# Optimization experiments

Measured on AMD Instinct MI355X. Metric: run time of the kernel, lower is better.

Reference implementation:

```python
import jax, jax.numpy as jnp
import numpy as np

B, NWORD, HID = 4, 24, 512


def setup_inputs() -> dict:
    key = jax.random.key(0)
    ks = jax.random.split(key, 7)
    H = HID
    scale_in = 1.0 / np.sqrt(H)
    return {
        "seqt": jax.random.normal(ks[0], (B, NWORD, 2 * H), dtype=jnp.float32),
        # ins_input_linearity: Linear(H -> 5H) with bias
        "Wi": jax.random.normal(ks[1], (5 * H, H), dtype=jnp.float32) * scale_in,
        "bi": jnp.zeros((5 * H,), dtype=jnp.float32),
        # ins_state_linearity: Linear(H -> 5H) with bias (bias init: forget slots = 1)
        "Ws": jax.random.normal(ks[2], (5 * H, H), dtype=jnp.float32) * scale_in,
        "bs": jnp.zeros((5 * H,), dtype=jnp.float32).at[H:2 * H].set(1.0),
        # ins_bilinearity: BilinearSimilarity(2H, 2H) -> scalar x^T W y
        "Wbil": jax.random.normal(ks[3], (2 * H, 2 * H), dtype=jnp.float32) * (1.0 / (2.0 * H)),
    }


def reference(seqt, Wi, bi, Ws, bs, Wbil):
    """Inside pass (do_inside) of DioLstm in training mode (soft_sum over splits).

    Chart cell (left, L) covers words [left, left+L]. Returns root v = concat(h, c).
    """
    Bn, n, twoH = seqt.shape
    H = twoH // 2
    # ins_bias buffer: ones on the two forget-gate slots [H:3H]
    ins_bias = jnp.zeros((5 * H,), dtype=seqt.dtype).at[H:3 * H].set(1.0)

    def single(seq):  # seq: [n, 2H]
        chartH = jnp.zeros((n, n, H), seq.dtype).at[:, 0].set(seq[:, :H])
        chartC = jnp.zeros((n, n, H), seq.dtype).at[:, 0].set(seq[:, H:])
        chartS = jnp.zeros((n, n), seq.dtype)  # leaf scores are 0
        for L in range(1, n):  # span length - 1 (static unroll over diagonals)
            P = n - L  # number of spans on this diagonal
            lefts = jnp.arange(P)[:, None]          # [P,1]
            ksplit = jnp.arange(L)[None, :]          # [1,L]
            # left child: (left, k); right child: (left+k+1, L-1-k)
            lH = chartH[lefts, ksplit]; lC = chartC[lefts, ksplit]; lS = chartS[lefts, ksplit]
            ridx = lefts + ksplit + 1
            rlen = jnp.broadcast_to(L - 1 - ksplit, ridx.shape)
            rH = chartH[ridx, rlen]; rC = chartC[ridx, rlen]; rS = chartS[ridx, rlen]
            lv = jnp.concatenate([lH, lC], axis=-1)  # [P,L,2H]
            rv = jnp.concatenate([rH, rC], axis=-1)
            # bilinear compatibility + child scores
            compat = jnp.einsum('pki,ij,pkj->pk', lv, Wbil, rv) + lS + rS  # [P,L]
            # projected_input + projected_state (sum once; gate slices of the sum)
            proj = (lH @ Wi.T + bi + ins_bias) + (rH @ Ws.T + bs)  # [P,L,5H]
            ig, lf, rf, g, og = jnp.split(proj, 5, axis=-1)
            ig = jax.nn.sigmoid(ig); lf = jax.nn.sigmoid(lf); rf = jax.nn.sigmoid(rf)
            g = jnp.tanh(g); og = jax.nn.sigmoid(og)
            mem = lf * lC + rf * rC + ig * g
            h = og * jnp.tanh(mem)  # [P,L,H]
            # soft_sum: torch.tensor(s_set) detaches scores -> stop_gradient on weights
            sw = jax.lax.stop_gradient(compat)
            w = jax.nn.softmax(sw, axis=-1)  # [P,L]
            Hnew = jnp.einsum('pk,pkh->ph', w, h)
            Cnew = jnp.einsum('pk,pkh->ph', w, mem)
            Snew = jnp.sum(w * sw, axis=-1)
            pidx = jnp.arange(P)
            chartH = chartH.at[pidx, L].set(Hnew)
            chartC = chartC.at[pidx, L].set(Cnew)
            chartS = chartS.at[pidx, L].set(Snew)
        # root cell v = concat(h, c)
        return jnp.concatenate([chartH[0, n - 1], chartC[0, n - 1]], axis=0)

    return jax.vmap(single)(seqt)  # [B, 2H]
```

## Files before the change

### kernel.cpp

```cpp
#include <hip/hip_runtime.h>
#include <math.h>

#define NB 4
#define NW 24
#define H 512
#define H2 1024
#define H5 2560
#define NCELL 300
#define NEED_BYTES ((size_t)72<<20)

static float* g_buf = nullptr;
__attribute__((constructor)) static void dio_alloc_ws(){
  (void)hipMalloc((void**)&g_buf, NEED_BYTES);
}

typedef __attribute__((ext_vector_type(8))) short bf16x8;
typedef __attribute__((ext_vector_type(4))) float f32x4;
typedef unsigned short ushort_t;

__device__ __forceinline__ int coff(int l){ return l*NW - (l*(l-1))/2; }
__device__ __forceinline__ float sigm(float x){ return 1.f/(1.f+__expf(-x)); }
__device__ __forceinline__ float ftanh(float x){ return 1.f - 2.f/(__expf(2.f*x)+1.f); }

__device__ __forceinline__ ushort_t f2b(float x){
  unsigned int u = __float_as_uint(x);
  u += 0x7FFF + ((u>>16)&1);
  return (ushort_t)(u>>16);
}
__device__ __forceinline__ float b2f(ushort_t h){
  return __uint_as_float(((unsigned int)h)<<16);
}
__device__ __forceinline__ void split_store(ushort_t* __restrict__ ph,
                                            ushort_t* __restrict__ pl,
                                            size_t idx, float x){
  ushort_t h = f2b(x);
  ph[idx] = h;
  pl[idx] = f2b(x - b2f(h));
}

__device__ __forceinline__ void gload_lds16(const void* g, void* l){
  __builtin_amdgcn_global_load_lds(
      (const __attribute__((address_space(1))) unsigned int*)g,
      (__attribute__((address_space(3))) unsigned int*)l, 16, 0, 0);
}

__device__ __forceinline__ float compat_dot(const float* __restrict__ cU,
                                            const float* __restrict__ cH,
                                            const float* __restrict__ cC,
                                            const float* __restrict__ cS,
                                            int lc, int rc, int lane){
  const float4* U4  = (const float4*)(cU + (size_t)lc*H2);
  const float4* Hr4 = (const float4*)(cH + (size_t)rc*H);
  const float4* Cr4 = (const float4*)(cC + (size_t)rc*H);
  float p = 0.f;
  #pragma unroll
  for (int it=0; it<2; it++){
    float4 u = U4[lane + 64*it], h = Hr4[lane + 64*it];
    p += u.x*h.x + u.y*h.y + u.z*h.z + u.w*h.w;
  }
  #pragma unroll
  for (int it=0; it<2; it++){
    float4 u = U4[128 + lane + 64*it], c = Cr4[lane + 64*it];
    p += u.x*c.x + u.y*c.y + u.z*c.z + u.w*c.w;
  }
  #pragma unroll
  for (int off=32; off>0; off>>=1) p += __shfl_down(p, off);
  return p + cS[lc] + cS[rc];
}

__global__ void k_init(const float* __restrict__ seqt,
                       const float* __restrict__ Wi, const float* __restrict__ Ws,
                       const float* __restrict__ Wbil,
                       ushort_t* __restrict__ WWblob, ushort_t* __restrict__ WBblob,
                       float* __restrict__ cH, float* __restrict__ cC, float* __restrict__ cS,
                       ushort_t* __restrict__ cHbh, ushort_t* __restrict__ cHbl,
                       ushort_t* __restrict__ cCbh, ushort_t* __restrict__ cCbl){
  const int blk = blockIdx.x, t = threadIdx.x;
  if (blk < 1280){
    const int gid = blk*256 + t;
    const int half = 163840;
    const float* mat = (gid < half) ? Wi : Ws;
    const int cid = (gid < half) ? gid : gid - half;
    const int j = cid >> 6;
    const int c0 = (cid & 63) << 3;
    const int tile = ((gid < half) ? 0 : 160) + (j >> 4);
    const int row = j & 15;
    const float4* s = (const float4*)(mat + (size_t)j*H + c0);
    float4 a = s[0], b4 = s[1];
    float xs[8] = {a.x,a.y,a.z,a.w, b4.x,b4.y,b4.z,b4.w};
    union { ushort_t u[8]; bf16x8 v; } hh, ll;
    #pragma unroll
    for (int i=0;i<8;i++){
      ushort_t h = f2b(xs[i]);
      hh.u[i] = h; ll.u[i] = f2b(xs[i] - b2f(h));
    }
    char* base = (char*)WWblob + (size_t)tile*32768;
    const int off = ((row<<10) + (c0<<1)) ^ ((row&7)<<4);
    *(bf16x8*)(base + off) = hh.v;
    *(bf16x8*)(base + 16384 + off) = ll.v;
  } else if (blk < 2304){
    __shared__ float tile[32][33];
    int tb = blk - 1280;
    int tr = (tb>>5)*32, tc = (tb&31)*32;
    int tx = t & 31, ty = t >> 5;
    #pragma unroll
    for (int i=0;i<32;i+=8)
      tile[ty+i][tx] = Wbil[(size_t)(tr+ty+i)*H2 + tc+tx];
    __syncthreads();
    if (t < 128){
      const int c = t & 31, r0 = (t >> 5) << 3;
      const int jg = tc + c;
      const int k0 = tr + r0;
      union { ushort_t u[8]; bf16x8 v; } hh, ll;
      #pragma unroll
      for (int i=0;i<8;i++){
        float x = tile[r0+i][c];
        ushort_t h = f2b(x);
        hh.u[i] = h; ll.u[i] = f2b(x - b2f(h));
      }
      char* base = (char*)WBblob + (size_t)(jg>>4)*65536;
      const int row = jg & 15;
      const int off = ((row<<11) + (k0<<1)) ^ ((row&7)<<4);
      *(bf16x8*)(base + off) = hh.v;
      *(bf16x8*)(base + 32768 + off) = ll.v;
    }
  } else {
    int tid = (blk-2304)*256 + t;
    if (tid < NB*NW*H){
      int b = tid/(NW*H); int r = tid%(NW*H); int i = r/H; int d = r%H;
      size_t idx = (size_t)(b*NCELL + i)*H + d;
      float hv = seqt[(size_t)(b*NW+i)*H2 + d];
      float cv = seqt[(size_t)(b*NW+i)*H2 + H + d];
      cH[idx]=hv; cC[idx]=cv;
      split_store(cHbh,cHbl,idx,hv);
      split_store(cCbh,cCbl,idx,cv);
      if (d==0) cS[b*NCELL+i] = 0.f;
    }
  }
}

__device__ __forceinline__ void mfma3(f32x4& acc, bf16x8 ah, bf16x8 al,
                                      bf16x8 bh, bf16x8 bl){
  acc = __builtin_amdgcn_mfma_f32_16x16x32_bf16(ah, bh, acc, 0,0,0);
  acc = __builtin_amdgcn_mfma_f32_16x16x32_bf16(ah, bl, acc, 0,0,0);
  acc = __builtin_amdgcn_mfma_f32_16x16x32_bf16(al, bh, acc, 0,0,0);
}

__global__ void __launch_bounds__(512)
k_proj4(const ushort_t* __restrict__ WWblob, const ushort_t* __restrict__ WBblob,
        const float* __restrict__ bi, const float* __restrict__ bs,
        const ushort_t* __restrict__ cHbh, const ushort_t* __restrict__ cHbl,
        const ushort_t* __restrict__ cCbh, const ushort_t* __restrict__ cCbl,
        const float* __restrict__ cC,
        float* __restrict__ cPI, float* __restrict__ cPS, float* __restrict__ cU,
        float* __restrict__ gH, float* __restrict__ gM,
        int d, int P)
{
  __shared__ __attribute__((aligned(16))) ushort_t wlds[32768];
  __shared__ f32x4 red[8][64];
  const int t = threadIdx.x, wv = t>>6, lane = t&63;
  const int jt = blockIdx.x;

  if (jt >= 384){
    const int Ln = d + 1;
    const int nk = Ln - 2;
    const int Pg = NW - Ln;
    const int gi = jt - 384;
    const int b = gi / (Pg*nk), rr = gi % (Pg*nk);
    const int left = rr / nk;
    const int k = 1 + rr % nk;
    const int lc = b*NCELL + coff(k) + left;
    const int rc = b*NCELL + coff(Ln-1-k) + left+k+1;
    const float* PI = cPI + (size_t)lc*H5;
    const float* PS = cPS + (size_t)rc*H5;
    const int dim = t;
    float p0 = PI[dim]     + PS[dim];
    float p1 = PI[H+dim]   + PS[H+dim];
    float p2 = PI[2*H+dim] + PS[2*H+dim];
    float p3 = PI[3*H+dim] + PS[3*H+dim];
    float p4 = PI[4*H+dim] + PS[4*H+dim];
    float lcv = cC[(size_t)lc*H + dim];
    float rcv = cC[(size_t)rc*H + dim];
    float mem = sigm(p1)*lcv + sigm(p2)*rcv + sigm(p0)*ftanh(p3);
    float h = sigm(p4)*ftanh(mem);
    const size_t gidx = ((size_t)(b*NW + left)*NW + k)*H + dim;
    gH[gidx] = h;
    gM[gidx] = mem;
    return;
  }

  const int r = lane & 15;
  const int q = lane >> 4;

  int kind, j0;
  if (jt < 160){ kind=0; j0 = jt*16; }
  else if (jt < 320){ kind=1; j0 = (jt-160)*16; }
  else { kind=2; j0 = (jt-320)*16; }

  {
    const char* blob = (kind < 2)
        ? (const char*)WWblob + (size_t)jt*32768
        : (const char*)WBblob + (size_t)(jt-320)*65536;
    const int nseg = (kind < 2) ? 4 : 8;
    for (int i = 0; i < nseg; i++){
      const int lo = i*8192 + wv*1024;
      gload_lds16(blob + lo + lane*16, (char*)wlds + lo);
    }
    asm volatile("s_waitcnt vmcnt(0)" ::: "memory");
  }
  __syncthreads();

  const int Mtot = NB*P, mt = (Mtot+15)>>4;
  const int swz = (r&7)<<4;
  const char* wb = (const char*)wlds;
  const int jo = j0 + r;
  float bias = 0.f;
  if (kind==0) bias = bi[jo] + ((jo>=H && jo<3*H)?1.f:0.f);
  else if (kind==1) bias = bs[jo];

  const f32x4 z4 = {0.f,0.f,0.f,0.f};
  const int units = 2*mt;
  const int rounds = (units + 7) >> 3;
  for (int rd = 0; rd < rounds; rd++){
    const int u = rd*8 + wv;
    const int half = u & 1;
    const int mtile = u >> 1;
    f32x4 sA = z4;
    int m0 = 0, nm = 0;
    if (u < units){
      m0 = mtile*16;
      nm = min(16, Mtot - m0);
      const int mg = m0 + (r < nm ? r : 0);
      const size_t arow = (size_t)((mg/P)*NCELL + coff(d) + mg%P)*H;
      f32x4 acc[4];
      #pragma unroll
      for (int wi=0;wi<4;wi++) acc[wi] = z4;
      if (kind < 2){
        #pragma unroll
        for (int wi=0; wi<4; wi++){
          const int w = half*4 + wi;
          #pragma unroll
          for (int s=0;s<2;s++){
            const int ko = w*64 + q*8 + s*32;
            bf16x8 ah = *(const bf16x8*)(cHbh + arow + ko);
            bf16x8 al = *(const bf16x8*)(cHbl + arow + ko);
            const int bo = ((r<<10) + (ko<<1)) ^ swz;
            bf16x8 bh = *(const bf16x8*)(wb + bo);
            bf16x8 bl = *(const bf16x8*)(wb + 16384 + bo);
            mfma3(acc[wi], ah, al, bh, bl);
          }
        }
      } else {
        const ushort_t* ah_ = (half==0 ? cHbh : cCbh) + arow;
        const ushort_t* al_ = (half==0 ? cHbl : cCbl) + arow;
        #pragma unroll
        for (int wi=0; wi<4; wi++){
          const int w = half*4 + wi;
          const int kg0 = w*128, ka0 = kg0 & 511;
          #pragma unroll
          for (int s=0;s<4;s++){
            const int so = s*32 + q*8;
            bf16x8 ah = *(const bf16x8*)(ah_ + ka0 + so);
            bf16x8 al = *(const bf16x8*)(al_ + ka0 + so);
            const int bo = ((r<<11) + ((kg0+so)<<1)) ^ swz;
            bf16x8 bh = *(const bf16x8*)(wb + bo);
            bf16x8 bl = *(const bf16x8*)(wb + 32768 + bo);
            mfma3(acc[wi], ah, al, bh, bl);
          }
        }
      }
      sA = (acc[0]+acc[1]) + (acc[2]+acc[3]);
    }
    red[wv][lane] = sA;
    __syncthreads();
    if (half==0 && u < units){
      f32x4 tot = red[wv][lane] + red[wv|1][lane];
      #pragma unroll
      for (int reg=0; reg<4; reg++){
        const int m = q*4 + reg;
        if (m < nm){
          const int mg2 = m0 + m;
          const size_t cell = (size_t)((mg2/P)*NCELL + coff(d) + mg2%P);
          const float v = tot[reg];
          if (kind==0)      cPI[cell*H5 + jo] = v + bias;
          else if (kind==1) cPS[cell*H5 + jo] = v + bias;
          else              cU [cell*H2 + jo] = v;
        }
      }
    }
    __syncthreads();
  }
}

__global__ void __launch_bounds__(512)
k_combine5(const float* __restrict__ cPI, const float* __restrict__ cPS,
           const float* __restrict__ cU,
           float* __restrict__ cH, float* __restrict__ cC, float* __restrict__ cS,
           ushort_t* __restrict__ cHbh, ushort_t* __restrict__ cHbl,
           ushort_t* __restrict__ cCbh, ushort_t* __restrict__ cCbl,
           const float* __restrict__ compatR, float* __restrict__ compatW,
           const float* __restrict__ gH, const float* __restrict__ gM,
           float* __restrict__ out, int L, int P){
  const int t = threadIdx.x;
  const int lane = t & 63;
  const int wave = t >> 6;
  const int ncomb = NB*P;
  const int blk = blockIdx.x;

  if (blk >= ncomb){
    const int P1 = P-1;
    const int nterm = L-1;
    int tid = (blk-ncomb)*8 + wave;
    if (P1 > 0 && nterm > 0 && tid < NB*P1*nterm){
      int cell1 = tid / nterm;
      int k = 1 + tid % nterm;
      int b = cell1 / P1, left = cell1 % P1;
      int lc = b*NCELL + coff(k) + left;
      int rc = b*NCELL + coff(L-k) + left+k+1;
      float v = compat_dot(cU, cH, cC, cS, lc, rc, lane);
      if (lane==0) compatW[(b*NW + left)*NW + k] = v;
    }
    return;
  }

  const int b = blk / P;
  const int left = blk % P;
  __shared__ float compat_s[32];
  __shared__ float wts_s[32];
  __shared__ float S_s;

  if (wave == 4){
    int lc = b*NCELL + left;
    int rc = b*NCELL + coff(L-1) + left+1;
    float v = compat_dot(cU, cH, cC, cS, lc, rc, lane);
    if (lane==0) compat_s[0] = v;
  } else if (wave == 5 && L >= 2){
    int lc = b*NCELL + coff(L-1) + left;
    int rc = b*NCELL + left+L;
    float v = compat_dot(cU, cH, cC, cS, lc, rc, lane);
    if (lane==0) compat_s[L-1] = v;
  }
  if (t >= 1 && t <= L-2) compat_s[t] = compatR[(b*NW + left)*NW + t];
  __syncthreads();
  if (t==0){
    float mx = -1e30f;
    for (int k=0;k<L;k++) mx = fmaxf(mx, compat_s[k]);
    float den = 0.f;
    for (int k=0;k<L;k++){ float e = __expf(compat_s[k]-mx); wts_s[k]=e; den+=e; }
    float inv = 1.f/den, S = 0.f;
    for (int k=0;k<L;k++){ wts_s[k]*=inv; S += wts_s[k]*compat_s[k]; }
    S_s = S;
  }
  __syncthreads();
  const int dim = t;
  float aH = 0.f, aC = 0.f;
  for (int q8=0; q8<8; q8++){
    float sH = 0.f, sC = 0.f;
    for (int k=q8; k<L; k+=8){
      float wk = wts_s[k];
      float mem, h;
      if (k == 0 || k == L-1){
        int lc = b*NCELL + coff(k) + left;
        int rc = b*NCELL + coff(L-1-k) + left+k+1;
        const float* PI = cPI + (size_t)lc*H5;
        const float* PS = cPS + (size_t)rc*H5;
        float p0 = PI[dim]     + PS[dim];
        float p1 = PI[H+dim]   + PS[H+dim];
        float p2 = PI[2*H+dim] + PS[2*H+dim];
        float p3 = PI[3*H+dim] + PS[3*H+dim];
        float p4 = PI[4*H+dim] + PS[4*H+dim];
        float lcv = cC[(size_t)lc*H + dim];
        float rcv = cC[(size_t)rc*H + dim];
        mem = sigm(p1)*lcv + sigm(p2)*rcv + sigm(p0)*ftanh(p3);
        h = sigm(p4)*ftanh(mem);
      } else {
        const size_t gidx = ((size_t)(b*NW + left)*NW + k)*H + dim;
        h = gH[gidx];
        mem = gM[gidx];
      }
      sH += wk*h; sC += wk*mem;
    }
    aH += sH; aC += sC;
  }
  if (L == NW-1){
    out[b*H2 + dim]     = aH;
    out[b*H2 + H + dim] = aC;
    return;
  }
  size_t nc = (size_t)(b*NCELL + coff(L) + left);
  cH[nc*H + dim] = aH;
  cC[nc*H + dim] = aC;
  split_store(cHbh,cHbl, nc*H + dim, aH);
  split_store(cCbh,cCbl, nc*H + dim, aC);
  if (t==0) cS[nc] = S_s;
}

extern "C" void kernel_launch(void* const* d_in, const int* in_sizes, int n_in,
                              void* d_out, int out_size, void* d_ws, size_t ws_size,
                              hipStream_t stream){
  const float* seqt = (const float*)d_in[0];
  const float* Wi   = (const float*)d_in[1];
  const float* bi   = (const float*)d_in[2];
  const float* Ws   = (const float*)d_in[3];
  const float* bs   = (const float*)d_in[4];
  const float* Wbil = (const float*)d_in[5];
  float* out = (float*)d_out;

  float* p = (ws_size >= NEED_BYTES && g_buf == nullptr) ? (float*)d_ws : g_buf;
  float* cH  = p; p += (size_t)NB*NCELL*H;
  float* cC  = p; p += (size_t)NB*NCELL*H;
  float* cS  = p; p += (size_t)NB*NCELL;
  float* cPI = p; p += (size_t)NB*NCELL*H5;
  float* cPS = p; p += (size_t)NB*NCELL*H5;
  float* cU  = p; p += (size_t)NB*NCELL*H2;
  float* compatA = p; p += (size_t)NB*NW*NW;
  float* compatB = p; p += (size_t)NB*NW*NW;
  float* gH  = p; p += (size_t)NB*NW*NW*H;
  float* gM  = p; p += (size_t)NB*NW*NW*H;
  ushort_t* u = (ushort_t*)p;
  ushort_t* WWblob = u; u += (size_t)320*16384;
  ushort_t* WBblob = u; u += (size_t)64*32768;
  ushort_t* cHbh   = u; u += (size_t)NB*NCELL*H;
  ushort_t* cHbl   = u; u += (size_t)NB*NCELL*H;
  ushort_t* cCbh   = u; u += (size_t)NB*NCELL*H;
  ushort_t* cCbl   = u; u += (size_t)NB*NCELL*H;

  k_init<<<2496, 256, 0, stream>>>(seqt, Wi, Ws, Wbil,
      WWblob, WBblob, cH, cC, cS, cHbh, cHbl, cCbh, cCbl);

  k_proj4<<<384, 512, 0, stream>>>(
      WWblob, WBblob, bi, bs,
      cHbh, cHbl, cCbh, cCbl, cC, cPI, cPS, cU, gH, gM, 0, NW);
  for (int L=1; L<NW; L++){
    int P = NW - L;
    int P1 = P-1, nterm = L-1;
    int wblk = (P1>0 && nterm>0) ? (NB*P1*nterm + 7)/8 : 0;
    float* bufR = (L&1) ? compatA : compatB;
    float* bufW = (L&1) ? compatB : compatA;
    k_combine5<<<NB*P + wblk, 512, 0, stream>>>(
        cPI, cPS, cU, cH, cC, cS, cHbh, cHbl, cCbh, cCbl,
        bufR, bufW, gH, gM, out, L, P);
    if (L < NW-1){
      int Ln = L + 1;
      int ngate = (Ln >= 3) ? NB*(NW-Ln)*(Ln-2) : 0;
      k_proj4<<<384 + ngate, 512, 0, stream>>>(
          WWblob, WBblob, bi, bs,
          cHbh, cHbl, cCbh, cCbl, cC, cPI, cPS, cU, gH, gM, L, P);
    }
  }
}
```

Before: 621.6 us.

## Fuse combine and projection stages into one kernel with atomic-counter handoff

Merges the per-diagonal combine kernel and the projection/gate/compat kernel into a single launch per stage. Projection blocks spin-wait on per-64-row atomic counters that the combine blocks bump after writing the new cells' bf16 hi/lo splits (now stored as packed 32-bit atomics). gH/gM become double-buffered so gate outputs for the next stage can be written while the current stage reads the previous ones. This roughly halves the number of launches and lets independent work overlap. The cost is spin-waiting that depends on combine blocks being scheduled first, and relaxed-ordering visibility assumptions between blocks.

```diff
diff --git a/kernel.cpp b/kernel.cpp
--- a/kernel.cpp
+++ b/kernel.cpp
@@ -7,7 +7,7 @@
 #define H2 1024
 #define H5 2560
 #define NCELL 300
-#define NEED_BYTES ((size_t)72<<20)
+#define NEED_BYTES ((size_t)80<<20)
 
 static float* g_buf = nullptr;
 __attribute__((constructor)) static void dio_alloc_ws(){
@@ -36,6 +36,16 @@
   ushort_t h = f2b(x);
   ph[idx] = h;
   pl[idx] = f2b(x - b2f(h));
+}
+
+__device__ __forceinline__ unsigned ldA(const unsigned* p){
+  return __hip_atomic_load(p, __ATOMIC_RELAXED, __HIP_MEMORY_SCOPE_AGENT);
+}
+__device__ __forceinline__ unsigned addA(unsigned* p, unsigned v){
+  return __hip_atomic_fetch_add(p, v, __ATOMIC_RELAXED, __HIP_MEMORY_SCOPE_AGENT);
+}
+__device__ __forceinline__ void stAu(unsigned* p, unsigned v){
+  __hip_atomic_store(p, v, __ATOMIC_RELAXED, __HIP_MEMORY_SCOPE_AGENT);
 }
 
 __device__ __forceinline__ void gload_lds16(const void* g, void* l){
@@ -74,7 +84,8 @@
                        ushort_t* __restrict__ WWblob, ushort_t* __restrict__ WBblob,
                        float* __restrict__ cH, float* __restrict__ cC, float* __restrict__ cS,
                        ushort_t* __restrict__ cHbh, ushort_t* __restrict__ cHbl,
-                       ushort_t* __restrict__ cCbh, ushort_t* __restrict__ cCbl){
+                       ushort_t* __restrict__ cCbh, ushort_t* __restrict__ cCbl,
+                       unsigned* __restrict__ ctr){
   const int blk = blockIdx.x, t = threadIdx.x;
   if (blk < 1280){
     const int gid = blk*256 + t;
@@ -124,7 +135,7 @@
       *(bf16x8*)(base + off) = hh.v;
       *(bf16x8*)(base + 32768 + off) = ll.v;
     }
-  } else {
+  } else if (blk < 2496){
     int tid = (blk-2304)*256 + t;
     if (tid < NB*NW*H){
       int b = tid/(NW*H); int r = tid%(NW*H); int i = r/H; int d = r%H;
@@ -136,6 +147,8 @@
       split_store(cCbh,cCbl,idx,cv);
       if (d==0) cS[b*NCELL+i] = 0.f;
     }
+  } else {
+    for (int i=t; i<NW*64; i+=256) ctr[i] = 0u;
   }
 }
 
@@ -147,48 +160,155 @@
 }
 
 __global__ void __launch_bounds__(512)
-k_proj4(const ushort_t* __restrict__ WWblob, const ushort_t* __restrict__ WBblob,
-        const float* __restrict__ bi, const float* __restrict__ bs,
-        const ushort_t* __restrict__ cHbh, const ushort_t* __restrict__ cHbl,
-        const ushort_t* __restrict__ cCbh, const ushort_t* __restrict__ cCbl,
-        const float* __restrict__ cC,
-        float* __restrict__ cPI, float* __restrict__ cPS, float* __restrict__ cU,
-        float* __restrict__ gH, float* __restrict__ gM,
-        int d, int P)
+k_stageF(const ushort_t* __restrict__ WWblob, const ushort_t* __restrict__ WBblob,
+         const float* __restrict__ bi, const float* __restrict__ bs,
+         ushort_t* __restrict__ cHbh, ushort_t* __restrict__ cHbl,
+         ushort_t* __restrict__ cCbh, ushort_t* __restrict__ cCbl,
+         float* __restrict__ cPI, float* __restrict__ cPS, float* __restrict__ cU,
+         float* __restrict__ cH, float* __restrict__ cC, float* __restrict__ cS,
+         const float* __restrict__ compatR, float* __restrict__ compatW,
+         const float* __restrict__ gHr, const float* __restrict__ gMr,
+         float* __restrict__ gHw, float* __restrict__ gMw,
+         unsigned* __restrict__ ctrL, float* __restrict__ out, int L, int P)
 {
   __shared__ __attribute__((aligned(16))) ushort_t wlds[32768];
   __shared__ f32x4 red[8][64];
+  __shared__ float compat_s[32];
+  __shared__ float wts_s[32];
+  __shared__ float S_s;
+
   const int t = threadIdx.x, wv = t>>6, lane = t&63;
-  const int jt = blockIdx.x;
-
-  if (jt >= 384){
-    const int Ln = d + 1;
-    const int nk = Ln - 2;
-    const int Pg = NW - Ln;
-    const int gi = jt - 384;
-    const int b = gi / (Pg*nk), rr = gi % (Pg*nk);
-    const int left = rr / nk;
-    const int k = 1 + rr % nk;
-    const int lc = b*NCELL + coff(k) + left;
-    const int rc = b*NCELL + coff(Ln-1-k) + left+k+1;
-    const float* PI = cPI + (size_t)lc*H5;
-    const float* PS = cPS + (size_t)rc*H5;
+  const int Mtot = NB*P;
+  const int ncomb = (L>=1) ? Mtot : 0;
+  const int nproj = (L<=NW-2) ? 384 : 0;
+  const int nk = L-1;
+  const int Pg = NW-L-1;
+  const int ngate = (nproj && nk>=1) ? NB*Pg*nk : 0;
+  int blk = blockIdx.x;
+
+  if (blk < ncomb){
+    const int b = blk / P, left = blk % P;
+    if (wv == 4){
+      int lc = b*NCELL + left;
+      int rc = b*NCELL + coff(L-1) + left+1;
+      float v = compat_dot(cU, cH, cC, cS, lc, rc, lane);
+      if (lane==0) compat_s[0] = v;
+    } else if (wv == 5 && L >= 2){
+      int lc = b*NCELL + coff(L-1) + left;
+      int rc = b*NCELL + left+L;
+      float v = compat_dot(cU, cH, cC, cS, lc, rc, lane);
+      if (lane==0) compat_s[L-1] = v;
+    }
+    if (t >= 1 && t <= L-2) compat_s[t] = compatR[(b*NW + left)*NW + t];
+    __syncthreads();
+    const size_t nc = (size_t)(b*NCELL + coff(L) + left);
+    if (t==0){
+      float mx = -1e30f;
+      for (int k=0;k<L;k++) mx = fmaxf(mx, compat_s[k]);
+      float den = 0.f;
+      for (int k=0;k<L;k++){ float e = __expf(compat_s[k]-mx); wts_s[k]=e; den+=e; }
+      float inv = 1.f/den, S = 0.f;
+      for (int k=0;k<L;k++){ wts_s[k]*=inv; S += wts_s[k]*compat_s[k]; }
+      if (L < NW-1) cS[nc] = S;
+    }
+    __syncthreads();
     const int dim = t;
-    float p0 = PI[dim]     + PS[dim];
-    float p1 = PI[H+dim]   + PS[H+dim];
-    float p2 = PI[2*H+dim] + PS[2*H+dim];
-    float p3 = PI[3*H+dim] + PS[3*H+dim];
-    float p4 = PI[4*H+dim] + PS[4*H+dim];
-    float lcv = cC[(size_t)lc*H + dim];
-    float rcv = cC[(size_t)rc*H + dim];
-    float mem = sigm(p1)*lcv + sigm(p2)*rcv + sigm(p0)*ftanh(p3);
-    float h = sigm(p4)*ftanh(mem);
-    const size_t gidx = ((size_t)(b*NW + left)*NW + k)*H + dim;
-    gH[gidx] = h;
-    gM[gidx] = mem;
+    float aH = 0.f, aC = 0.f;
+    for (int q8=0; q8<8; q8++){
+      float sH = 0.f, sC = 0.f;
+      for (int k=q8; k<L; k+=8){
+        float wk = wts_s[k];
+        float mem, h;
+        if (k == 0 || k == L-1){
+          int lc = b*NCELL + coff(k) + left;
+          int rc = b*NCELL + coff(L-1-k) + left+k+1;
+          const float* PI = cPI + (size_t)lc*H5;
+          const float* PS = cPS + (size_t)rc*H5;
+          float p0 = PI[dim]     + PS[dim];
+          float p1 = PI[H+dim]   + PS[H+dim];
+          float p2 = PI[2*H+dim] + PS[2*H+dim];
+          float p3 = PI[3*H+dim] + PS[3*H+dim];
+          float p4 = PI[4*H+dim] + PS[4*H+dim];
+          float lcv = cC[(size_t)lc*H + dim];
+          float rcv = cC[(size_t)rc*H + dim];
+          mem = sigm(p1)*lcv + sigm(p2)*rcv + sigm(p0)*ftanh(p3);
+          h = sigm(p4)*ftanh(mem);
+        } else {
+          const size_t gidx = ((size_t)(b*NW + left)*NW + k)*H + dim;
+          h = gHr[gidx];
+          mem = gMr[gidx];
+        }
+        sH += wk*h; sC += wk*mem;
+      }
+      aH += sH; aC += sC;
+    }
+    if (L == NW-1){
+      out[b*H2 + dim]     = aH;
+      out[b*H2 + H + dim] = aC;
+      return;
+    }
+    cH[nc*H + dim] = aH;
+    cC[nc*H + dim] = aC;
+    ushort_t hH = f2b(aH), lH = f2b(aH - b2f(hH));
+    ushort_t hC = f2b(aC), lC = f2b(aC - b2f(hC));
+    unsigned nh = (unsigned)__shfl_down((int)hH, 1);
+    unsigned nl = (unsigned)__shfl_down((int)lH, 1);
+    unsigned mh = (unsigned)__shfl_down((int)hC, 1);
+    unsigned ml = (unsigned)__shfl_down((int)lC, 1);
+    if (!(t & 1)){
+      const size_t pi = (nc*H + dim) >> 1;
+      stAu((unsigned*)cHbh + pi, (unsigned)hH | (nh<<16));
+      stAu((unsigned*)cHbl + pi, (unsigned)lH | (nl<<16));
+      stAu((unsigned*)cCbh + pi, (unsigned)hC | (mh<<16));
+      stAu((unsigned*)cCbl + pi, (unsigned)lC | (ml<<16));
+    }
+    __syncthreads();
+    if (t == 0) addA(ctrL + ((blk>>6)<<5), 1u);
     return;
   }
-
+  blk -= ncomb;
+
+  if (blk >= nproj){
+    const int gi = blk - nproj;
+    if (gi < ngate){
+      const int Ln = L + 1;
+      const int b = gi / (Pg*nk), rr = gi % (Pg*nk);
+      const int left = rr / nk;
+      const int k = 1 + rr % nk;
+      const int lc = b*NCELL + coff(k) + left;
+      const int rc = b*NCELL + coff(Ln-1-k) + left+k+1;
+      const float* PI = cPI + (size_t)lc*H5;
+      const float* PS = cPS + (size_t)rc*H5;
+      const int dim = t;
+      float p0 = PI[dim]     + PS[dim];
+      float p1 = PI[H+dim]   + PS[H+dim];
+      float p2 = PI[2*H+dim] + PS[2*H+dim];
+      float p3 = PI[3*H+dim] + PS[3*H+dim];
+      float p4 = PI[4*H+dim] + PS[4*H+dim];
+      float lcv = cC[(size_t)lc*H + dim];
+      float rcv = cC[(size_t)rc*H + dim];
+      float mem = sigm(p1)*lcv + sigm(p2)*rcv + sigm(p0)*ftanh(p3);
+      float h = sigm(p4)*ftanh(mem);
+      const size_t gidx = ((size_t)(b*NW + left)*NW + k)*H + dim;
+      gHw[gidx] = h;
+      gMw[gidx] = mem;
+    } else {
+      const int Ln = L + 1;
+      const int tid8 = (gi - ngate)*8 + wv;
+      if (tid8 < NB*Pg*nk){
+        const int cell1 = tid8 / nk;
+        const int k = 1 + tid8 % nk;
+        const int b = cell1 / Pg, left = cell1 % Pg;
+        const int lc = b*NCELL + coff(k) + left;
+        const int rc = b*NCELL + coff(Ln-1-k) + left+k+1;
+        float v = compat_dot(cU, cH, cC, cS, lc, rc, lane);
+        if (lane==0) compatW[(b*NW + left)*NW + k] = v;
+      }
+    }
+    return;
+  }
+
+  const int jt = blk;
   const int r = lane & 15;
   const int q = lane >> 4;
 
@@ -210,7 +330,7 @@
   }
   __syncthreads();
 
-  const int Mtot = NB*P, mt = (Mtot+15)>>4;
+  const int mt = (Mtot+15)>>4;
   const int swz = (r&7)<<4;
   const char* wb = (const char*)wlds;
   const int jo = j0 + r;
@@ -222,6 +342,14 @@
   const int units = 2*mt;
   const int rounds = (units + 7) >> 3;
   for (int rd = 0; rd < rounds; rd++){
+    if (ncomb > 0){
+      if (t == 0){
+        const int c0 = rd*64;
+        const unsigned tgt = (unsigned)((Mtot - c0 < 64) ? (Mtot - c0) : 64);
+        while (ldA(ctrL + (rd<<5)) < tgt) __builtin_amdgcn_s_sleep(8);
+      }
+      __syncthreads();
+    }
     const int u = rd*8 + wv;
     const int half = u & 1;
     const int mtile = u >> 1;
@@ -231,7 +359,7 @@
       m0 = mtile*16;
       nm = min(16, Mtot - m0);
       const int mg = m0 + (r < nm ? r : 0);
-      const size_t arow = (size_t)((mg/P)*NCELL + coff(d) + mg%P)*H;
+      const size_t arow = (size_t)((mg/P)*NCELL + coff(L) + mg%P)*H;
       f32x4 acc[4];
       #pragma unroll
       for (int wi=0;wi<4;wi++) acc[wi] = z4;
@@ -280,7 +408,7 @@
         const int m = q*4 + reg;
         if (m < nm){
           const int mg2 = m0 + m;
-          const size_t cell = (size_t)((mg2/P)*NCELL + coff(d) + mg2%P);
+          const size_t cell = (size_t)((mg2/P)*NCELL + coff(L) + mg2%P);
           const float v = tot[reg];
           if (kind==0)      cPI[cell*H5 + jo] = v + bias;
           else if (kind==1) cPS[cell*H5 + jo] = v + bias;
@@ -290,109 +418,6 @@
     }
     __syncthreads();
   }
-}
-
-__global__ void __launch_bounds__(512)
-k_combine5(const float* __restrict__ cPI, const float* __restrict__ cPS,
-           const float* __restrict__ cU,
-           float* __restrict__ cH, float* __restrict__ cC, float* __restrict__ cS,
-           ushort_t* __restrict__ cHbh, ushort_t* __restrict__ cHbl,
-           ushort_t* __restrict__ cCbh, ushort_t* __restrict__ cCbl,
-           const float* __restrict__ compatR, float* __restrict__ compatW,
-           const float* __restrict__ gH, const float* __restrict__ gM,
-           float* __restrict__ out, int L, int P){
-  const int t = threadIdx.x;
-  const int lane = t & 63;
-  const int wave = t >> 6;
-  const int ncomb = NB*P;
-  const int blk = blockIdx.x;
-
-  if (blk >= ncomb){
-    const int P1 = P-1;
-    const int nterm = L-1;
-    int tid = (blk-ncomb)*8 + wave;
-    if (P1 > 0 && nterm > 0 && tid < NB*P1*nterm){
-      int cell1 = tid / nterm;
-      int k = 1 + tid % nterm;
-      int b = cell1 / P1, left = cell1 % P1;
-      int lc = b*NCELL + coff(k) + left;
-      int rc = b*NCELL + coff(L-k) + left+k+1;
-      float v = compat_dot(cU, cH, cC, cS, lc, rc, lane);
-      if (lane==0) compatW[(b*NW + left)*NW + k] = v;
-    }
-    return;
-  }
-
-  const int b = blk / P;
-  const int left = blk % P;
-  __shared__ float compat_s[32];
-  __shared__ float wts_s[32];
-  __shared__ float S_s;
-
-  if (wave == 4){
-    int lc = b*NCELL + left;
-    int rc = b*NCELL + coff(L-1) + left+1;
-    float v = compat_dot(cU, cH, cC, cS, lc, rc, lane);
-    if (lane==0) compat_s[0] = v;
-  } else if (wave == 5 && L >= 2){
-    int lc = b*NCELL + coff(L-1) + left;
-    int rc = b*NCELL + left+L;
-    float v = compat_dot(cU, cH, cC, cS, lc, rc, lane);
-    if (lane==0) compat_s[L-1] = v;
-  }
-  if (t >= 1 && t <= L-2) compat_s[t] = compatR[(b*NW + left)*NW + t];
-  __syncthreads();
-  if (t==0){
-    float mx = -1e30f;
-    for (int k=0;k<L;k++) mx = fmaxf(mx, compat_s[k]);
-    float den = 0.f;
-    for (int k=0;k<L;k++){ float e = __expf(compat_s[k]-mx); wts_s[k]=e; den+=e; }
-    float inv = 1.f/den, S = 0.f;
-    for (int k=0;k<L;k++){ wts_s[k]*=inv; S += wts_s[k]*compat_s[k]; }
-    S_s = S;
-  }
-  __syncthreads();
-  const int dim = t;
-  float aH = 0.f, aC = 0.f;
-  for (int q8=0; q8<8; q8++){
-    float sH = 0.f, sC = 0.f;
-    for (int k=q8; k<L; k+=8){
-      float wk = wts_s[k];
-      float mem, h;
-      if (k == 0 || k == L-1){
-        int lc = b*NCELL + coff(k) + left;
-        int rc = b*NCELL + coff(L-1-k) + left+k+1;
-        const float* PI = cPI + (size_t)lc*H5;
-        const float* PS = cPS + (size_t)rc*H5;
-        float p0 = PI[dim]     + PS[dim];
-        float p1 = PI[H+dim]   + PS[H+dim];
-        float p2 = PI[2*H+dim] + PS[2*H+dim];
-        float p3 = PI[3*H+dim] + PS[3*H+dim];
-        float p4 = PI[4*H+dim] + PS[4*H+dim];
-        float lcv = cC[(size_t)lc*H + dim];
-        float rcv = cC[(size_t)rc*H + dim];
-        mem = sigm(p1)*lcv + sigm(p2)*rcv + sigm(p0)*ftanh(p3);
-        h = sigm(p4)*ftanh(mem);
-      } else {
-        const size_t gidx = ((size_t)(b*NW + left)*NW + k)*H + dim;
-        h = gH[gidx];
-        mem = gM[gidx];
-      }
-      sH += wk*h; sC += wk*mem;
-    }
-    aH += sH; aC += sC;
-  }
-  if (L == NW-1){
-    out[b*H2 + dim]     = aH;
-    out[b*H2 + H + dim] = aC;
-    return;
-  }
-  size_t nc = (size_t)(b*NCELL + coff(L) + left);
-  cH[nc*H + dim] = aH;
-  cC[nc*H + dim] = aC;
-  split_store(cHbh,cHbl, nc*H + dim, aH);
-  split_store(cCbh,cCbl, nc*H + dim, aC);
-  if (t==0) cS[nc] = S_s;
 }
 
 extern "C" void kernel_launch(void* const* d_in, const int* in_sizes, int n_in,
@@ -415,8 +440,10 @@
   float* cU  = p; p += (size_t)NB*NCELL*H2;
   float* compatA = p; p += (size_t)NB*NW*NW;
   float* compatB = p; p += (size_t)NB*NW*NW;
-  float* gH  = p; p += (size_t)NB*NW*NW*H;
-  float* gM  = p; p += (size_t)NB*NW*NW*H;
+  float* gHa = p; p += (size_t)NB*NW*NW*H;
+  float* gMa = p; p += (size_t)NB*NW*NW*H;
+  float* gHb = p; p += (size_t)NB*NW*NW*H;
+  float* gMb = p; p += (size_t)NB*NW*NW*H;
   ushort_t* u = (ushort_t*)p;
   ushort_t* WWblob = u; u += (size_t)320*16384;
   ushort_t* WBblob = u; u += (size_t)64*32768;
@@ -424,28 +451,27 @@
   ushort_t* cHbl   = u; u += (size_t)NB*NCELL*H;
   ushort_t* cCbh   = u; u += (size_t)NB*NCELL*H;
   ushort_t* cCbl   = u; u += (size_t)NB*NCELL*H;
-
-  k_init<<<2496, 256, 0, stream>>>(seqt, Wi, Ws, Wbil,
-      WWblob, WBblob, cH, cC, cS, cHbh, cHbl, cCbh, cCbl);
-
-  k_proj4<<<384, 512, 0, stream>>>(
-      WWblob, WBblob, bi, bs,
-      cHbh, cHbl, cCbh, cCbl, cC, cPI, cPS, cU, gH, gM, 0, NW);
-  for (int L=1; L<NW; L++){
-    int P = NW - L;
-    int P1 = P-1, nterm = L-1;
-    int wblk = (P1>0 && nterm>0) ? (NB*P1*nterm + 7)/8 : 0;
-    float* bufR = (L&1) ? compatA : compatB;
-    float* bufW = (L&1) ? compatB : compatA;
-    k_combine5<<<NB*P + wblk, 512, 0, stream>>>(
-        cPI, cPS, cU, cH, cC, cS, cHbh, cHbl, cCbh, cCbl,
-        bufR, bufW, gH, gM, out, L, P);
-    if (L < NW-1){
-      int Ln = L + 1;
-      int ngate = (Ln >= 3) ? NB*(NW-Ln)*(Ln-2) : 0;
-      k_proj4<<<384 + ngate, 512, 0, stream>>>(
-          WWblob, WBblob, bi, bs,
-          cHbh, cHbl, cCbh, cCbl, cC, cPI, cPS, cU, gH, gM, L, P);
-    }
-  }
-}
+  unsigned* ctr    = (unsigned*)u;
+
+  k_init<<<2497, 256, 0, stream>>>(seqt, Wi, Ws, Wbil,
+      WWblob, WBblob, cH, cC, cS, cHbh, cHbl, cCbh, cCbl, ctr);
+
+  for (int L = 0; L < NW; L++){
+    const int P = NW - L;
+    const int ncomb = (L>=1) ? NB*P : 0;
+    const int nproj = (L<=NW-2) ? 384 : 0;
+    const int Ln = L + 1, nk = L - 1, Pg = NW - Ln;
+    const int ngate = (nproj && nk>=1) ? NB*Pg*nk : 0;
+    const int wblk  = (nproj && nk>=1) ? (NB*Pg*nk + 7)/8 : 0;
+    float* bufR = (L&1)  ? compatA : compatB;
+    float* bufW = (Ln&1) ? compatA : compatB;
+    const float* gHr = (L&1)  ? gHa : gHb;
+    const float* gMr = (L&1)  ? gMa : gMb;
+    float* gHw = (Ln&1) ? gHa : gHb;
+    float* gMw = (Ln&1) ? gMa : gMb;
+    k_stageF<<<ncomb + nproj + ngate + wblk, 512, 0, stream>>>(
+        WWblob, WBblob, bi, bs,
+        cHbh, cHbl, cCbh, cCbl, cPI, cPS, cU, cH, cC, cS,
+        bufR, bufW, gHr, gMr, gHw, gMw, ctr + L*64, out, L, P);
+  }
+}
```

After: 668.8 us. +7.6%, slower.
